# Kernel optimization log

Hardware: AMD Instinct MI355X
Metric: run time of the kernel (lower is better)

## Reference

```python
import jax, jax.numpy as jnp
import numpy as np


def _rel_dist(h, w, dtype):
    # cell-centered unit grid in [0,1], mapped to [-1,1]
    ys = (jnp.arange(h, dtype=dtype) + 0.5) / h
    xs = (jnp.arange(w, dtype=dtype) + 0.5) / w
    gy, gx = jnp.meshgrid(ys, xs, indexing='ij')     # (h, w)
    coords = 2.0 * jnp.stack([gy, gx], axis=-1) - 1.0  # (h, w, 2)
    c1 = coords[None, None, :, :, :]   # (1,1,h,w,2)  -> h2,w2
    c2 = coords[:, :, None, None, :]   # (h,w,1,1,2)  -> h1,w1
    return jnp.tanh(2.0 * (c1 - c2))   # (h1,w1,h2,w2,2)


def setup_inputs() -> dict:
    key = jax.random.key(0)
    ks = jax.random.split(key, 6)
    B, Ci, Co, H, W = 16, 16, 16, 24, 24
    hidden = 64
    v = jax.random.normal(ks[0], (B, Ci, H, W), dtype=jnp.float32)
    w1 = jax.random.normal(ks[1], (hidden, 2), dtype=jnp.float32) * (1.0 / np.sqrt(2.0))
    b1 = jax.random.normal(ks[2], (hidden,), dtype=jnp.float32) * 0.02
    w2 = jax.random.normal(ks[3], (Co * Ci, hidden), dtype=jnp.float32) * (1.0 / np.sqrt(hidden))
    b2 = jax.random.normal(ks[4], (Co * Ci,), dtype=jnp.float32) * 0.02
    bias = jax.random.normal(ks[5], (Co, 1, 1), dtype=jnp.float32) * (1.0 / np.sqrt(Ci))
    return {"v": v, "w1": w1, "b1": b1, "w2": w2, "b2": b2, "bias": bias}


def reference(v, w1, b1, w2, b2, bias):
    H, W = v.shape[-2], v.shape[-1]
    Co, Ci = bias.shape[0], v.shape[-3]
    rel = _rel_dist(H, W, v.dtype)                       # (h1,w1,h2,w2,2)
    hid = jax.nn.gelu(rel @ w1.T + b1, approximate=False)  # (h1,w1,h2,w2,64)
    kernel = (hid @ w2.T + b2).reshape(H, W, H, W, Co, Ci)  # (h1,w1,h2,w2,o,i)
    out = jnp.einsum('hwHWoi,biHW->bohw', kernel, v) / (H * W)
    return out + bias
```

## Files before the change

### kernel.cpp

```cpp
#include <hip/hip_runtime.h>
#include <hip/hip_bf16.h>


typedef __attribute__((ext_vector_type(8))) short bf16x8;
typedef __attribute__((ext_vector_type(4))) float f32x4;

#define KT_ELEMS (47*49*256)
#define VPAD2_ELEMS (40*40*256)
#define NROWS (47*49)
#define NPOS 576
#define NOCT 7
#define PREP_BUILD_BLOCKS 288
#define PREP_PAD_BLOCKS (VPAD2_ELEMS/256)

__launch_bounds__(256)
__global__ void prep(const float* __restrict__ v,
                     const float* __restrict__ w1, const float* __restrict__ b1,
                     const float* __restrict__ w2, const float* __restrict__ b2,
                     __hip_bfloat16* __restrict__ kt, __hip_bfloat16* __restrict__ vpad)
{
    const int tid = threadIdx.x;

    if (blockIdx.x >= PREP_BUILD_BLOCKS) {
        int idx = (blockIdx.x - PREP_BUILD_BLOCKS)*256 + tid;
        if (idx >= VPAD2_ELEMS) return;
        int i = idx & 15;
        int b = (idx >> 4) & 15;
        int s = idx >> 8;
        int x = s % 40;
        int y = s / 40;
        int h = y - 8, w = x - 8;
        float val = 0.0f;
        if (h >= 0 && h < 24 && w >= 0 && w < 24)
            val = v[((b*16 + i)*24 + h)*24 + w];
        vpad[idx] = __float2bfloat16(val);
        return;
    }

    __shared__ float ty_s[47];
    __shared__ float tx_s[49];
    __shared__ float hid_s[8][64];
    const int r0 = blockIdx.x * 8;

    if (tid < 47)               ty_s[tid]      = tanhf((float)(tid - 23) * (1.0f/6.0f));
    if (tid >= 64 && tid < 113) tx_s[tid - 64] = tanhf((float)(tid - 64 - 24) * (1.0f/6.0f));
    __syncthreads();

    #pragma unroll
    for (int k = 0; k < 2; ++k) {
        int idx = k*256 + tid;
        int rr  = idx >> 6;
        int j   = idx & 63;
        int r   = r0 + rr;
        if (r >= NROWS) r = NROWS - 1;
        int dy47 = r / 49;
        int dxi  = r % 49;
        float x = ty_s[dy47]*w1[2*j] + tx_s[dxi]*w1[2*j+1] + b1[j];
        hid_s[rr][j] = 0.5f*x*(1.0f + erff(x*0.70710678118f));
    }
    __syncthreads();

    const int c = tid;
    float acc[8];
    const float bb = b2[c];
    #pragma unroll
    for (int r = 0; r < 8; ++r) acc[r] = bb;

    const float4* w2v = (const float4*)w2;
    #pragma unroll
    for (int jv = 0; jv < 16; ++jv) {
        float4 wv = w2v[c*16 + jv];
        #pragma unroll
        for (int e = 0; e < 4; ++e) {
            float we = ((const float*)&wv)[e];
            int j = jv*4 + e;
            #pragma unroll
            for (int r = 0; r < 8; ++r)
                acc[r] += hid_s[r][j] * we;
        }
    }

    #pragma unroll
    for (int rr = 0; rr < 8; ++rr) {
        int r = r0 + rr;
        if (r >= NROWS) break;
        kt[r*256 + c] = __float2bfloat16(acc[rr]);
    }
}

__launch_bounds__(512, 8)
__global__ void conv_part(const __hip_bfloat16* __restrict__ kt_,
                          const __hip_bfloat16* __restrict__ vpad_,
                          float* __restrict__ part)
{
    __shared__ f32x4 red[8][4][64];
    const short* kt = (const short*)kt_;
    const short* vp = (const short*)vpad_;

    const int w   = blockIdx.x;
    const int hg  = blockIdx.y;
    const int oct = blockIdx.z;
    const int h0  = hg * 4;

    const int tid  = threadIdx.x;
    const int lane = tid & 63;
    const int wv   = tid >> 6;
    const int tq   = wv & 3;
    const int dxh  = wv >> 2;
    const int n    = lane & 15;
    const int g    = lane >> 4;
    const int d    = g >> 1;
    const int ih   = (g & 1) * 8;

    const int t = oct*4 + tq;

    f32x4 acc[4];
    #pragma unroll
    for (int hh = 0; hh < 4; ++hh) acc[hh] = (f32x4){0.f,0.f,0.f,0.f};

    if (t < 27) {
        const int dy47 = t - h0 + 20;
        const short* ap = kt + ((long)(dy47*49 + (24 - w + 12*dxh + d)))*256 + n*16 + ih;
        const short* bp = vp + ((long)((t + 5)*40 + (8 + 12*dxh + d)))*256 + n*16 + ih;
        #pragma unroll
        for (int p = 0; p < 6; ++p) {
            bf16x8 av = *(const bf16x8*)(ap + p*512);
            #pragma unroll
            for (int hh = 0; hh < 4; ++hh) {
                bf16x8 bv = *(const bf16x8*)(bp + hh*10240 + p*512);
                acc[hh] = __builtin_amdgcn_mfma_f32_16x16x32_bf16(av, bv, acc[hh], 0, 0, 0);
            }
        }
    }

    #pragma unroll
    for (int hh = 0; hh < 4; ++hh) red[wv][hh][lane] = acc[hh];
    __syncthreads();

    if (wv < 4) {
        f32x4 s = red[0][wv][lane];
        #pragma unroll
        for (int src = 1; src < 8; ++src) s += red[src][wv][lane];

        const int p = (h0 + wv)*24 + w;
        float* dst = part + ((size_t)oct*NPOS + p)*256 + (n*16 + g*4);
        *(f32x4*)dst = s;
    }
}

__launch_bounds__(256)
__global__ void combine(const float* __restrict__ part, const float* __restrict__ bias,
                        float* __restrict__ out)
{
    __shared__ float lds[16][257];
    const int tid = threadIdx.x;
    const int p0  = blockIdx.x * 16;

    #pragma unroll
    for (int pp = 0; pp < 16; ++pp) {
        float s = 0.f;
        #pragma unroll
        for (int oct = 0; oct < NOCT; ++oct)
            s += part[((size_t)oct*NPOS + p0 + pp)*256 + tid];
        lds[pp][tid] = s;
    }
    __syncthreads();

    const int pp = tid & 15;
    const int g  = tid >> 4;
    const float sc = 1.0f/576.0f;
    #pragma unroll
    for (int cc = 0; cc < 16; ++cc) {
        int c2 = cc*16 + g;
        out[(size_t)c2*576 + p0 + pp] = lds[pp][c2]*sc + bias[c2 & 15];
    }
}

extern "C" void kernel_launch(void* const* d_in, const int* in_sizes, int n_in,
                              void* d_out, int out_size, void* d_ws, size_t ws_size,
                              hipStream_t stream)
{
    const float* v    = (const float*)d_in[0];
    const float* w1   = (const float*)d_in[1];
    const float* b1   = (const float*)d_in[2];
    const float* w2   = (const float*)d_in[3];
    const float* b2   = (const float*)d_in[4];
    const float* bias = (const float*)d_in[5];
    float* out = (float*)d_out;

    char* ws = (char*)d_ws;
    __hip_bfloat16* kt   = (__hip_bfloat16*)ws;
    __hip_bfloat16* vpad = (__hip_bfloat16*)(ws + (size_t)KT_ELEMS*2);
    float* part = (float*)(ws + (size_t)KT_ELEMS*2 + (size_t)VPAD2_ELEMS*2);

    prep<<<dim3(PREP_BUILD_BLOCKS + PREP_PAD_BLOCKS), dim3(256), 0, stream>>>(
        v, w1, b1, w2, b2, kt, vpad);
    conv_part<<<dim3(24, 6, NOCT), dim3(512), 0, stream>>>(kt, vpad, part);
    combine<<<dim3(NPOS/16), dim3(256), 0, stream>>>(part, bias, out);
}
```

Measured before the change: 28.08 us.

## Register-tile conv_part over four output columns with sliding kernel-row reuse

Each conv block now computes a 4-wide by 4-tall output tile instead of a single column, so the grid shrinks from 24 to 6 blocks along width. Waves split the output rows into pairs, and kernel A-fragments are kept in a four-register sliding window across the dx loop so each A load is reused by four output columns. The goal is fewer redundant global loads of kernel and input data. The cost is fewer blocks (252 total), more accumulator registers, and a two-pass LDS reduction with an extra barrier. The launch-bounds occupancy hint is also dropped.

```diff
diff --git a/kernel.cpp b/kernel.cpp
--- a/kernel.cpp
+++ b/kernel.cpp
@@ -88,7 +88,7 @@
     }
 }
 
-__launch_bounds__(512, 8)
+__launch_bounds__(512)
 __global__ void conv_part(const __hip_bfloat16* __restrict__ kt_,
                           const __hip_bfloat16* __restrict__ vpad_,
                           float* __restrict__ part)
@@ -97,16 +97,17 @@
     const short* kt = (const short*)kt_;
     const short* vp = (const short*)vpad_;
 
-    const int w   = blockIdx.x;
+    const int wt  = blockIdx.x;
     const int hg  = blockIdx.y;
     const int oct = blockIdx.z;
+    const int w0  = wt * 4;
     const int h0  = hg * 4;
 
     const int tid  = threadIdx.x;
     const int lane = tid & 63;
     const int wv   = tid >> 6;
     const int tq   = wv & 3;
-    const int dxh  = wv >> 2;
+    const int hhh  = wv >> 2;
     const int n    = lane & 15;
     const int g    = lane >> 4;
     const int d    = g >> 1;
@@ -114,35 +115,59 @@
 
     const int t = oct*4 + tq;
 
-    f32x4 acc[4];
-    #pragma unroll
-    for (int hh = 0; hh < 4; ++hh) acc[hh] = (f32x4){0.f,0.f,0.f,0.f};
+    f32x4 acc[2][4];
+    #pragma unroll
+    for (int hh = 0; hh < 2; ++hh)
+        #pragma unroll
+        for (int ww = 0; ww < 4; ++ww) acc[hh][ww] = (f32x4){0.f,0.f,0.f,0.f};
 
     if (t < 27) {
         const int dy47 = t - h0 + 20;
-        const short* ap = kt + ((long)(dy47*49 + (24 - w + 12*dxh + d)))*256 + n*16 + ih;
-        const short* bp = vp + ((long)((t + 5)*40 + (8 + 12*dxh + d)))*256 + n*16 + ih;
-        #pragma unroll
-        for (int p = 0; p < 6; ++p) {
-            bf16x8 av = *(const bf16x8*)(ap + p*512);
+        const short* apb = kt + ((long)(dy47*49 + (24 - w0 + d)))*256 + n*16 + ih;
+        const short* bpb = vp + ((long)((t + hhh*2 + 5)*40 + (8 + d)))*256 + n*16 + ih;
+
+        bf16x8 av[4];
+        av[0] = *(const bf16x8*)(apb);
+        av[1] = *(const bf16x8*)(apb - 256);
+        av[2] = *(const bf16x8*)(apb - 512);
+        av[3] = *(const bf16x8*)(apb - 768);
+
+        #pragma unroll
+        for (int dxp = 0; dxp < 12; ++dxp) {
+            bf16x8 bv0 = *(const bf16x8*)(bpb +         dxp*512);
+            bf16x8 bv1 = *(const bf16x8*)(bpb + 10240 + dxp*512);
             #pragma unroll
-            for (int hh = 0; hh < 4; ++hh) {
-                bf16x8 bv = *(const bf16x8*)(bp + hh*10240 + p*512);
-                acc[hh] = __builtin_amdgcn_mfma_f32_16x16x32_bf16(av, bv, acc[hh], 0, 0, 0);
+            for (int ww = 0; ww < 4; ++ww) {
+                acc[0][ww] = __builtin_amdgcn_mfma_f32_16x16x32_bf16(av[ww], bv0, acc[0][ww], 0, 0, 0);
+                acc[1][ww] = __builtin_amdgcn_mfma_f32_16x16x32_bf16(av[ww], bv1, acc[1][ww], 0, 0, 0);
+            }
+            if (dxp < 11) {
+                av[2] = av[0];
+                av[3] = av[1];
+                av[0] = *(const bf16x8*)(apb + (2*dxp + 2)*256);
+                av[1] = *(const bf16x8*)(apb + (2*dxp + 1)*256);
             }
         }
     }
 
     #pragma unroll
-    for (int hh = 0; hh < 4; ++hh) red[wv][hh][lane] = acc[hh];
-    __syncthreads();
-
-    if (wv < 4) {
-        f32x4 s = red[0][wv][lane];
-        #pragma unroll
-        for (int src = 1; src < 8; ++src) s += red[src][wv][lane];
-
-        const int p = (h0 + wv)*24 + w;
+    for (int hh = 0; hh < 2; ++hh) {
+        if (hh) __syncthreads();
+        #pragma unroll
+        for (int ww = 0; ww < 4; ++ww) red[wv][ww][lane] = acc[hh][ww];
+        __syncthreads();
+
+        const int hhh2 = wv >> 2;
+        const int ww2  = wv & 3;
+        f32x4 s = red[0 + 0][ww2][lane];
+        s = red[4*hhh2 + 0][ww2][lane];
+        s += red[4*hhh2 + 1][ww2][lane];
+        s += red[4*hhh2 + 2][ww2][lane];
+        s += red[4*hhh2 + 3][ww2][lane];
+
+        const int h = h0 + hhh2*2 + hh;
+        const int w = w0 + ww2;
+        const int p = h*24 + w;
         float* dst = part + ((size_t)oct*NPOS + p)*256 + (n*16 + g*4);
         *(f32x4*)dst = s;
     }
@@ -195,6 +220,6 @@
 
     prep<<<dim3(PREP_BUILD_BLOCKS + PREP_PAD_BLOCKS), dim3(256), 0, stream>>>(
         v, w1, b1, w2, b2, kt, vpad);
-    conv_part<<<dim3(24, 6, NOCT), dim3(512), 0, stream>>>(kt, vpad, part);
+    conv_part<<<dim3(6, 6, NOCT), dim3(512), 0, stream>>>(kt, vpad, part);
     combine<<<dim3(NPOS/16), dim3(256), 0, stream>>>(part, bias, out);
 }
```

Result: faster. 25.39 us (-9.6%).

## Fuse conv partial sums and combine into a single direct conv kernel

Applied to the files above, without the earlier changes.

Replaces the split-K conv kernel (7 octants writing partial sums to global memory) plus the separate combine kernel with one kernel. Each block handles one output row and four adjacent output columns, iterating over all kernel rows across 8 waves with 3 steps each. It reuses the loaded v tiles across four output columns by sliding the kernel-row registers. The final reduction, scaling and bias add now happen in LDS inside the same kernel. This removes a kernel launch and the global round trip of the partial sums, but the grid shrinks to 144 blocks and each wave does a longer serial MFMA chain, which may reduce parallelism.

```diff
diff --git a/kernel.cpp b/kernel.cpp
--- a/kernel.cpp
+++ b/kernel.cpp
@@ -9,7 +9,6 @@
 #define VPAD2_ELEMS (40*40*256)
 #define NROWS (47*49)
 #define NPOS 576
-#define NOCT 7
 #define PREP_BUILD_BLOCKS 288
 #define PREP_PAD_BLOCKS (VPAD2_ELEMS/256)
 
@@ -88,91 +87,93 @@
     }
 }
 
-__launch_bounds__(512, 8)
-__global__ void conv_part(const __hip_bfloat16* __restrict__ kt_,
-                          const __hip_bfloat16* __restrict__ vpad_,
-                          float* __restrict__ part)
+__launch_bounds__(512)
+__global__ void conv_direct(const __hip_bfloat16* __restrict__ kt_,
+                            const __hip_bfloat16* __restrict__ vpad_,
+                            const float* __restrict__ bias,
+                            float* __restrict__ out)
 {
     __shared__ f32x4 red[8][4][64];
     const short* kt = (const short*)kt_;
     const short* vp = (const short*)vpad_;
 
-    const int w   = blockIdx.x;
-    const int hg  = blockIdx.y;
-    const int oct = blockIdx.z;
-    const int h0  = hg * 4;
+    const int wt = blockIdx.x;
+    const int h  = blockIdx.y;
+    const int w0 = wt * 4;
 
     const int tid  = threadIdx.x;
     const int lane = tid & 63;
     const int wv   = tid >> 6;
-    const int tq   = wv & 3;
-    const int dxh  = wv >> 2;
     const int n    = lane & 15;
     const int g    = lane >> 4;
     const int d    = g >> 1;
     const int ih   = (g & 1) * 8;
 
-    const int t = oct*4 + tq;
-
     f32x4 acc[4];
     #pragma unroll
-    for (int hh = 0; hh < 4; ++hh) acc[hh] = (f32x4){0.f,0.f,0.f,0.f};
+    for (int ww = 0; ww < 4; ++ww) acc[ww] = (f32x4){0.f,0.f,0.f,0.f};
 
-    if (t < 27) {
-        const int dy47 = t - h0 + 20;
-        const short* ap = kt + ((long)(dy47*49 + (24 - w + 12*dxh + d)))*256 + n*16 + ih;
-        const short* bp = vp + ((long)((t + 5)*40 + (8 + 12*dxh + d)))*256 + n*16 + ih;
+    #pragma unroll
+    for (int k = 0; k < 3; ++k) {
+        const int t = wv + k*8;
+        const int dy47 = t - h + 23;
+        const short* apb = kt + ((long)(dy47*49 + (24 - w0 + d)))*256 + n*16 + ih;
+        const short* bpb = vp + ((long)((t + 8)*40 + (8 + d)))*256 + n*16 + ih;
+
+        bf16x8 bv[12];
         #pragma unroll
-        for (int p = 0; p < 6; ++p) {
-            bf16x8 av = *(const bf16x8*)(ap + p*512);
+        for (int dxp = 0; dxp < 12; ++dxp)
+            bv[dxp] = *(const bf16x8*)(bpb + dxp*512);
+
+        bf16x8 av[4];
+        av[0] = *(const bf16x8*)(apb);
+        av[1] = *(const bf16x8*)(apb - 256);
+        av[2] = *(const bf16x8*)(apb - 512);
+        av[3] = *(const bf16x8*)(apb - 768);
+
+        #pragma unroll
+        for (int dxp = 0; dxp < 12; ++dxp) {
             #pragma unroll
-            for (int hh = 0; hh < 4; ++hh) {
-                bf16x8 bv = *(const bf16x8*)(bp + hh*10240 + p*512);
-                acc[hh] = __builtin_amdgcn_mfma_f32_16x16x32_bf16(av, bv, acc[hh], 0, 0, 0);
+            for (int ww = 0; ww < 4; ++ww)
+                acc[ww] = __builtin_amdgcn_mfma_f32_16x16x32_bf16(av[ww], bv[dxp], acc[ww], 0, 0, 0);
+            if (dxp < 11) {
+                av[2] = av[0];
+                av[3] = av[1];
+                av[0] = *(const bf16x8*)(apb + (2*dxp + 2)*256);
+                av[1] = *(const bf16x8*)(apb + (2*dxp + 1)*256);
             }
         }
     }
 
     #pragma unroll
-    for (int hh = 0; hh < 4; ++hh) red[wv][hh][lane] = acc[hh];
+    for (int ww = 0; ww < 4; ++ww) red[wv][ww][lane] = acc[ww];
     __syncthreads();
 
+    f32x4 s;
     if (wv < 4) {
-        f32x4 s = red[0][wv][lane];
+        s = red[0][wv][lane];
         #pragma unroll
         for (int src = 1; src < 8; ++src) s += red[src][wv][lane];
-
-        const int p = (h0 + wv)*24 + w;
-        float* dst = part + ((size_t)oct*NPOS + p)*256 + (n*16 + g*4);
-        *(f32x4*)dst = s;
-    }
-}
-
-__launch_bounds__(256)
-__global__ void combine(const float* __restrict__ part, const float* __restrict__ bias,
-                        float* __restrict__ out)
-{
-    __shared__ float lds[16][257];
-    const int tid = threadIdx.x;
-    const int p0  = blockIdx.x * 16;
-
-    #pragma unroll
-    for (int pp = 0; pp < 16; ++pp) {
-        float s = 0.f;
-        #pragma unroll
-        for (int oct = 0; oct < NOCT; ++oct)
-            s += part[((size_t)oct*NPOS + p0 + pp)*256 + tid];
-        lds[pp][tid] = s;
     }
     __syncthreads();
 
-    const int pp = tid & 15;
-    const int g  = tid >> 4;
-    const float sc = 1.0f/576.0f;
-    #pragma unroll
-    for (int cc = 0; cc < 16; ++cc) {
-        int c2 = cc*16 + g;
-        out[(size_t)c2*576 + p0 + pp] = lds[pp][c2]*sc + bias[c2 & 15];
+    float* lds2 = (float*)red;
+    if (wv < 4) {
+        const int c2b = n*16 + g*4;
+        #pragma unroll
+        for (int e = 0; e < 4; ++e) lds2[wv*256 + c2b + e] = s[e];
+    }
+    __syncthreads();
+
+    if (tid < 256) {
+        const float sc = 1.0f/576.0f;
+        const float bb = bias[tid & 15];
+        float4 o;
+        o.x = lds2[0*256 + tid]*sc + bb;
+        o.y = lds2[1*256 + tid]*sc + bb;
+        o.z = lds2[2*256 + tid]*sc + bb;
+        o.w = lds2[3*256 + tid]*sc + bb;
+        *(float4*)(out + (size_t)tid*NPOS + h*24 + w0) = o;
     }
 }
 
@@ -191,10 +192,8 @@
     char* ws = (char*)d_ws;
     __hip_bfloat16* kt   = (__hip_bfloat16*)ws;
     __hip_bfloat16* vpad = (__hip_bfloat16*)(ws + (size_t)KT_ELEMS*2);
-    float* part = (float*)(ws + (size_t)KT_ELEMS*2 + (size_t)VPAD2_ELEMS*2);
 
     prep<<<dim3(PREP_BUILD_BLOCKS + PREP_PAD_BLOCKS), dim3(256), 0, stream>>>(
         v, w1, b1, w2, b2, kt, vpad);
-    conv_part<<<dim3(24, 6, NOCT), dim3(512), 0, stream>>>(kt, vpad, part);
-    combine<<<dim3(NPOS/16), dim3(256), 0, stream>>>(part, bias, out);
+    conv_direct<<<dim3(6, 24), dim3(512), 0, stream>>>(kt, vpad, bias, out);
 }
```

Result: slower. 29.50 us (+5.1%).
